# Kernel optimization log

Measured on AMD Instinct MI355X. Metric: run time of the kernel, lower is better.

## Reference

```python
import jax, jax.numpy as jnp
import numpy as np
from jax import lax

B, T, H, W = 4, 8, 14, 14
DIM, NH = 768, 8
HD = DIM // NH            # 96, head dim (= depthwise conv channels)
G = 1                     # global_embed_num
N = T * H * W + 1 + G     # 1570 tokens: [global, cls, spatial]
HID = 4 * DIM
BIG = 1.0e8


def ln(x, g, b, eps=1e-5):
    m = jnp.mean(x, axis=-1, keepdims=True)
    v = jnp.mean(jnp.square(x - m), axis=-1, keepdims=True)
    return (x - m) * jax.lax.rsqrt(v + eps) * g + b


def setup_inputs() -> dict:
    key = jax.random.key(0)
    ks = jax.random.split(key, 12)
    s = 0.02
    inp = {
        "x": jax.random.normal(ks[0], (B, N, DIM), jnp.float32),
        "t": T, "h": H, "w": W,
        "norm1_g": jnp.ones((DIM,), jnp.float32),
        "norm1_b": jnp.zeros((DIM,), jnp.float32),
        "qkv_w": jax.random.normal(ks[1], (3 * DIM, DIM), jnp.float32) * s,
        "qkv_b": jnp.zeros((3 * DIM,), jnp.float32),
        "conv_q": jax.random.normal(ks[2], (HD, 1, 3, 3, 3), jnp.float32) * 0.05,
        "nq_g": jnp.ones((HD,), jnp.float32), "nq_b": jnp.zeros((HD,), jnp.float32),
        "conv_k": jax.random.normal(ks[3], (HD, 1, 3, 3, 3), jnp.float32) * 0.05,
        "nk_g": jnp.ones((HD,), jnp.float32), "nk_b": jnp.zeros((HD,), jnp.float32),
        "conv_v": jax.random.normal(ks[4], (HD, 1, 3, 3, 3), jnp.float32) * 0.05,
        "nv_g": jnp.ones((HD,), jnp.float32), "nv_b": jnp.zeros((HD,), jnp.float32),
        "proj_w": jax.random.normal(ks[5], (DIM, DIM), jnp.float32) * s,
        "proj_b": jnp.zeros((DIM,), jnp.float32),
        "norm2_g": jnp.ones((DIM,), jnp.float32),
        "norm2_b": jnp.zeros((DIM,), jnp.float32),
        "fc1_w": jax.random.normal(ks[6], (HID, DIM), jnp.float32) * s,
        "fc1_b": jnp.zeros((HID,), jnp.float32),
        "fc2_w": jax.random.normal(ks[7], (DIM, HID), jnp.float32) * s,
        "fc2_b": jnp.zeros((DIM,), jnp.float32),
    }
    return inp


def _pool(tok, cw, g, b):
    # tok: [B, NH, N, HD] -> depthwise conv3d per head on spatial tokens, then LN
    glob, cls, body = tok[:, :, :G], tok[:, :, G:G + 1], tok[:, :, G + 1:]
    z = body.reshape(B * NH, T, H, W, HD).transpose(0, 4, 1, 2, 3)  # [BN, C, T, H, W]
    z = lax.conv_general_dilated(z, cw, window_strides=(1, 1, 1),
                                 padding=[(1, 1)] * 3, feature_group_count=HD,
                                 dimension_numbers=("NCDHW", "OIDHW", "NCDHW"))
    z = z.reshape(B, NH, HD, T * H * W).transpose(0, 1, 3, 2)       # [B, NH, L, HD]
    z = jnp.concatenate([glob, cls, z], axis=2)                     # splice cls then global
    return ln(z, g, b)


def reference(x, t, h, w, norm1_g, norm1_b, qkv_w, qkv_b,
              conv_q, nq_g, nq_b, conv_k, nk_g, nk_b, conv_v, nv_g, nv_b,
              proj_w, proj_b, norm2_g, norm2_b, fc1_w, fc1_b, fc2_w, fc2_b):
    scale = HD ** (-0.5)
    xn = ln(x, norm1_g, norm1_b)
    qkv = (xn @ qkv_w.T + qkv_b).reshape(B, N, 3, NH, HD)
    qkv = qkv.transpose(2, 0, 3, 1, 4)            # [3, B, NH, N, HD]
    q = _pool(qkv[0], conv_q, nq_g, nq_b)
    k = _pool(qkv[1], conv_k, nk_g, nk_b)
    v = _pool(qkv[2], conv_v, nv_g, nv_b)

    attn = jnp.einsum("bhnd,bhmd->bhnm", q, k) * scale
    # additive offset: BIG everywhere except diagonal and the global columns (rows >= G)
    eye = jnp.eye(N, dtype=attn.dtype)
    off2 = eye * BIG
    off2 = off2.at[G:, :G].set(BIG)
    offset = BIG - off2                            # [N, N]
    attn = jax.nn.softmax(attn - offset, axis=-1)

    o = jnp.einsum("bhnm,bhmd->bhnd", attn, v)     # [B, NH, N, HD]
    o = o.transpose(0, 2, 1, 3).reshape(B, N, DIM)
    o = o @ proj_w.T + proj_b

    x = x + o                                      # pool_skip is None -> identity skip
    x2 = ln(x, norm2_g, norm2_b)
    mlp = jax.nn.gelu(x2 @ fc1_w.T + fc1_b, approximate=False) @ fc2_w.T + fc2_b
    return x + mlp
```

## Files before the change

### kernel.cpp

```cpp
#include <hip/hip_runtime.h>
#include <hip/hip_bf16.h>
#include <cmath>

using bf16 = __hip_bfloat16;
using bf16x8_t = __attribute__((ext_vector_type(8))) short;
using f32x4_t  = __attribute__((ext_vector_type(4))) float;

constexpr int kT = 8;
constexpr int kDIM = 768, kNH = 8, kHD = 96;
constexpr int kN = 1570;
constexpr int kB = 4;
constexpr int kM = kB * kN;
constexpr int kBNH = kB * kNH;
constexpr long kPoolRows  = (long)kBNH * kN;
constexpr long kPoolElems = kPoolRows * kHD;

struct SegTab { const void* src[22]; long start[23]; };

__global__ void detect_kernel(const unsigned* __restrict__ probe,
                              unsigned* __restrict__ flag) {
  *flag = (probe[0] == 0x3F803F80u) ? 1u : 0u;
}

__global__ void convert_kernel(SegTab tab, bf16* __restrict__ cin,
                               const unsigned* __restrict__ flag, long chunks) {
  const bool isb = (*flag != 0u);
  const long stride = (long)gridDim.x * blockDim.x;
  for (long c = (long)blockIdx.x * blockDim.x + threadIdx.x; c < chunks; c += stride) {
    const long e8 = c * 8;
    int lo = 0, hi = 22;
    while (hi - lo > 1) { int mid = (lo + hi) >> 1; if (e8 >= tab.start[mid]) lo = mid; else hi = mid; }
    const long e = e8 - tab.start[lo];
    if (isb) {
      *(bf16x8_t*)(cin + e8) = *(const bf16x8_t*)((const unsigned short*)tab.src[lo] + e);
    } else {
      const float* s = (const float*)tab.src[lo] + e;
      float4 a = *(const float4*)s;
      float4 b = *(const float4*)(s + 4);
      bf16 r[8];
      r[0] = (bf16)a.x; r[1] = (bf16)a.y; r[2] = (bf16)a.z; r[3] = (bf16)a.w;
      r[4] = (bf16)b.x; r[5] = (bf16)b.y; r[6] = (bf16)b.z; r[7] = (bf16)b.w;
      *(bf16x8_t*)(cin + e8) = *(bf16x8_t*)r;
    }
  }
}

__device__ __forceinline__ void gload_lds16(const bf16* g, bf16* l) {
  __builtin_amdgcn_global_load_lds(
      (const __attribute__((address_space(1))) unsigned int*)g,
      (__attribute__((address_space(3))) unsigned int*)l, 16, 0, 0);
}

template<int EPI, int DUAL>
__launch_bounds__(256, 2)
__global__ void gemm_bt(const bf16* __restrict__ A, const bf16* __restrict__ Wt,
                        const bf16* __restrict__ bias, const bf16* __restrict__ res,
                        bf16* __restrict__ C, float* __restrict__ Cf,
                        const unsigned* __restrict__ flagp,
                        int M, int K, int Nout, int tiles_n)
{
  __shared__ bf16 shm[32768];
  const int tid  = threadIdx.x;
  const int lane = tid & 63;
  const int wv   = tid >> 6;
  const int wr   = wv >> 1, wc = wv & 1;

  const int nwg = gridDim.x;
  const int q8 = nwg >> 3, r8 = nwg & 7;
  const int xcd = blockIdx.x & 7, slot = blockIdx.x >> 3;
  const int base = (xcd < r8) ? xcd * (q8 + 1) : r8 * (q8 + 1) + (xcd - r8) * q8;
  const int lin = base + slot;
  const int grp = lin / (2 * tiles_n);
  const int rem = lin - grp * 2 * tiles_n;
  const long tile_m = (long)(grp * 2 + (rem & 1)) * 128;
  const long tile_n = (long)(rem >> 1) * 128;

  bool isb = true;
  if constexpr (DUAL) isb = (*flagp != 0u);

  f32x4_t zero = {0.f, 0.f, 0.f, 0.f};
  f32x4_t acc[4][4];
#pragma unroll
  for (int i = 0; i < 4; ++i)
#pragma unroll
    for (int j = 0; j < 4; ++j) acc[i][j] = zero;

  const int rbase = tid >> 3;
  const int g8 = (((tid & 7) ^ (rbase & 7))) * 8;
  const bf16* srcA[4];
  const bf16* srcB[4];
#pragma unroll
  for (int i = 0; i < 4; ++i) {
    long ar = tile_m + i * 32 + rbase; if (ar > M - 1) ar = M - 1;
    srcA[i] = A  + ar * K + g8;
    srcB[i] = Wt + (tile_n + i * 32 + rbase) * K + g8;
  }

  auto stage = [&](int kt, int buf) {
    const long koff = (long)kt << 6;
    bf16* ab = shm + buf * 8192;
    bf16* bp = shm + 16384 + buf * 8192;
#pragma unroll
    for (int i = 0; i < 4; ++i)
      gload_lds16(srcA[i] + koff, ab + i * 2048 + wv * 512);
#pragma unroll
    for (int i = 0; i < 4; ++i)
      gload_lds16(srcB[i] + koff, bp + i * 2048 + wv * 512);
  };

  const int qq = lane & 7;
  const int j0 = (((lane >> 4) ^ qq)) * 8;
  const int j1 = (((lane >> 4) ^ 4 ^ qq)) * 8;
  const int rA = wr * 64 + (lane & 15);
  const int rB = wc * 64 + (lane & 15);

  const int ksteps = K >> 6;
  stage(0, 0);
  stage(1, 1);
  asm volatile("s_waitcnt vmcnt(8)" ::: "memory");
  __builtin_amdgcn_s_barrier();

#define KSTEP(BUF, DOPF, PFKT)                                                 \
  {                                                                            \
    const bf16* ab = shm + (BUF) * 8192;                                       \
    const bf16* bp = shm + 16384 + (BUF) * 8192;                               \
    bf16x8_t a[4][2], bfr[4][2];                                               \
    _Pragma("unroll")                                                          \
    for (int m = 0; m < 4; ++m) {                                              \
      a[m][0]   = *(const bf16x8_t*)&ab[((rA + m * 16) << 6) + j0];            \
      a[m][1]   = *(const bf16x8_t*)&ab[((rA + m * 16) << 6) + j1];            \
      bfr[m][0] = *(const bf16x8_t*)&bp[((rB + m * 16) << 6) + j0];            \
      bfr[m][1] = *(const bf16x8_t*)&bp[((rB + m * 16) << 6) + j1];            \
    }                                                                          \
    asm volatile("s_waitcnt lgkmcnt(0)" ::: "memory");                         \
    __builtin_amdgcn_sched_barrier(0);                                         \
    __builtin_amdgcn_s_barrier();                                              \
    if (DOPF) stage((PFKT), (BUF));                                            \
    __builtin_amdgcn_s_setprio(1);                                             \
    _Pragma("unroll")                                                          \
    for (int m = 0; m < 4; ++m)                                                \
      _Pragma("unroll")                                                        \
      for (int n = 0; n < 4; ++n) {                                            \
        acc[m][n] = __builtin_amdgcn_mfma_f32_16x16x32_bf16(a[m][0], bfr[n][0], acc[m][n], 0, 0, 0); \
        acc[m][n] = __builtin_amdgcn_mfma_f32_16x16x32_bf16(a[m][1], bfr[n][1], acc[m][n], 0, 0, 0); \
      }                                                                        \
    __builtin_amdgcn_s_setprio(0);                                             \
    if (DOPF) { asm volatile("s_waitcnt vmcnt(8)" ::: "memory"); }             \
    else      { asm volatile("s_waitcnt vmcnt(0)" ::: "memory"); }             \
    __builtin_amdgcn_s_barrier();                                              \
  }

  for (int p = 0; p < ksteps; p += 2) {
    KSTEP(0, p + 2 < ksteps, p + 2)
    KSTEP(1, p + 3 < ksteps, p + 3)
  }
#undef KSTEP

  {
    const int colB = wc * 64 + (lane & 15);
    const int rowB = wr * 64 + ((lane >> 4) << 2);
#pragma unroll
    for (int n = 0; n < 4; ++n) {
      const int col = colB + n * 16;
      const float bv = (float)bias[tile_n + col];
#pragma unroll
      for (int m = 0; m < 4; ++m)
#pragma unroll
        for (int r = 0; r < 4; ++r)
          shm[(rowB + m * 16 + r) * 136 + col] = (bf16)(acc[m][n][r] + bv);
    }
  }
  __syncthreads();
#pragma unroll
  for (int c8 = 0; c8 < 8; ++c8) {
    const int chunk = tid + c8 * 256;
    const int row = chunk >> 4;
    const int colc = (chunk & 15) * 8;
    const long grow = tile_m + row;
    if (grow < M) {
      const bf16x8_t v8 = *(const bf16x8_t*)&shm[row * 136 + colc];
      const long gcol = tile_n + colc;
      float f[8];
#pragma unroll
      for (int j = 0; j < 8; ++j) {
        unsigned short u = (unsigned short)v8[j];
        f[j] = __uint_as_float((unsigned)u << 16);
      }
      if constexpr (EPI == 1) {
#pragma unroll
        for (int j = 0; j < 8; ++j) {
          const float v2 = f[j];
          const float zarg = 1.59576912160573f * v2 * (1.f + 0.044715f * v2 * v2);
          f[j] = v2 * __builtin_amdgcn_rcpf(1.f + __expf(-zarg));
        }
      } else if constexpr (EPI == 2) {
        const bf16x8_t rv = *(const bf16x8_t*)&res[grow * Nout + gcol];
#pragma unroll
        for (int j = 0; j < 8; ++j) {
          unsigned short u = (unsigned short)rv[j];
          f[j] += __uint_as_float((unsigned)u << 16);
        }
      }
      if (DUAL && !isb) {
        float4 s0 = {f[0], f[1], f[2], f[3]};
        float4 s1 = {f[4], f[5], f[6], f[7]};
        *(float4*)&Cf[grow * Nout + gcol] = s0;
        *(float4*)&Cf[grow * Nout + gcol + 4] = s1;
      } else {
        bf16 o8[8];
#pragma unroll
        for (int j = 0; j < 8; ++j) o8[j] = (bf16)f[j];
        *(bf16x8_t*)&C[grow * Nout + gcol] = *(bf16x8_t*)o8;
      }
    }
  }
}

__global__ void ln768_kernel(const bf16* __restrict__ x, const bf16* __restrict__ g,
                             const bf16* __restrict__ bta, bf16* __restrict__ y)
{
  const long row = blockIdx.x;
  const int tid = threadIdx.x;
  const bf16* xr = x + row * kDIM;
  float v[3];
  float s = 0.f, ss = 0.f;
#pragma unroll
  for (int i = 0; i < 3; ++i) {
    v[i] = (float)xr[tid + i * 256];
    s += v[i]; ss += v[i] * v[i];
  }
#pragma unroll
  for (int off = 32; off; off >>= 1) {
    s  += __shfl_xor(s, off);
    ss += __shfl_xor(ss, off);
  }
  __shared__ float red[8];
  const int wv = tid >> 6;
  if ((tid & 63) == 0) { red[wv] = s; red[4 + wv] = ss; }
  __syncthreads();
  s  = red[0] + red[1] + red[2] + red[3];
  ss = red[4] + red[5] + red[6] + red[7];
  const float mean = s * (1.f / kDIM);
  const float var  = ss * (1.f / kDIM) - mean * mean;
  const float rstd = rsqrtf(var + 1e-5f);
  bf16* yr = y + row * kDIM;
#pragma unroll
  for (int i = 0; i < 3; ++i) {
    const int c = tid + i * 256;
    yr[c] = (bf16)((v[i] - mean) * rstd * (float)g[c] + (float)bta[c]);
  }
}

__launch_bounds__(256, 2)
__global__ void convpool2_kernel(const bf16* __restrict__ qkv,
                                 const bf16* __restrict__ cwq,
                                 const bf16* __restrict__ cwk,
                                 const bf16* __restrict__ cwv,
                                 bf16* __restrict__ pool)
{
  __shared__ bf16 tile[3 * 256 * 40];
  const int t    = blockIdx.x;
  const int bh   = blockIdx.y;
  const int z    = blockIdx.z;
  const int s    = z / 3, cgrp = z - s * 3;
  const int tid  = threadIdx.x;
  const int b    = bh >> 3, h = bh & 7;

  const bf16* src0 = qkv + (long)(b * kN) * 2304 + s * kDIM + h * kHD + cgrp * 32;

  {
    f32x4_t z4 = {0.f, 0.f, 0.f, 0.f};
    for (int i = tid; i < 3840; i += 256)
      *(f32x4_t*)((char*)tile + (long)i * 16) = z4;
  }
  __syncthreads();

  for (int c = tid; c < 2352; c += 256) {
    const int slice = c / 784;
    const int rem   = c - slice * 784;
    const int p     = rem >> 2;
    const int seg   = rem & 3;
    const int tt    = t + slice - 1;
    if ((unsigned)tt < 8u) {
      const int y = p / 14, x = p - y * 14;
      const int n = 2 + tt * 196 + p;
      const bf16x8_t v = *(const bf16x8_t*)(src0 + (long)n * 2304 + seg * 8);
      *(bf16x8_t*)((char*)tile + ((long)(slice * 256 + (y + 1) * 16 + (x + 1)) * 40 + seg * 8) * 2) = v;
    }
  }

  const int dpair = tid & 15;
  const int pg    = tid >> 4;
  const int d0    = cgrp * 32 + dpair * 2;
  const bf16* cw  = (s == 0) ? cwq : (s == 1) ? cwk : cwv;
  float w0[27], w1[27];
#pragma unroll
  for (int i = 0; i < 27; ++i) {
    w0[i] = (float)cw[d0 * 27 + i];
    w1[i] = (float)cw[(d0 + 1) * 27 + i];
  }
  __syncthreads();

  bf16* out0 = pool + (long)s * kPoolElems + (long)bh * kN * kHD;
  for (int p = pg; p < 196; p += 16) {
    const int y = p / 14, x = p - y * 14;
    const char* bp = (const char*)tile + ((long)(y * 16 + x) * 40 + dpair * 2) * 2;
    float a0 = 0.f, a1 = 0.f;
#pragma unroll
    for (int dt = 0; dt < 3; ++dt)
#pragma unroll
      for (int dy = 0; dy < 3; ++dy)
#pragma unroll
        for (int dx = 0; dx < 3; ++dx) {
          const unsigned u = *(const unsigned*)(bp + dt * 20480 + dy * 1280 + dx * 80);
          const int i = (dt * 3 + dy) * 3 + dx;
          a0 = fmaf(__uint_as_float(u << 16), w0[i], a0);
          a1 = fmaf(__uint_as_float(u & 0xffff0000u), w1[i], a1);
        }
    const int n = 2 + t * 196 + p;
    bf16 r0 = (bf16)a0, r1 = (bf16)a1;
    unsigned pk = ((unsigned)*(unsigned short*)&r1 << 16) | *(unsigned short*)&r0;
    *(unsigned*)((char*)(out0 + (long)n * kHD + d0)) = pk;
  }
  if (t == 0 && tid < 64) {
    const int tok = tid >> 5, dd = tid & 31;
    out0[(long)tok * kHD + cgrp * 32 + dd] = src0[(long)tok * 2304 + dd];
  }
}

__global__ void ln96_kernel(bf16* __restrict__ pool,
                            const bf16* __restrict__ gq, const bf16* __restrict__ bq,
                            const bf16* __restrict__ gk, const bf16* __restrict__ bk,
                            const bf16* __restrict__ gv, const bf16* __restrict__ bv)
{
  const int z = blockIdx.y;
  bf16* buf = pool + (long)z * kPoolElems;
  const bf16* g  = (z == 0) ? gq : (z == 1) ? gk : gv;
  const bf16* be = (z == 0) ? bq : (z == 1) ? bk : bv;
  const long row = (long)blockIdx.x * 4 + (threadIdx.x >> 6);
  if (row >= kPoolRows) return;
  const int lane = threadIdx.x & 63;
  bf16* p = buf + row * kHD;
  float a0 = 0.f, a1 = 0.f;
  if (lane < 48) {
    a0 = (float)p[lane * 2];
    a1 = (float)p[lane * 2 + 1];
  }
  float sSum = a0 + a1, sSq = a0 * a0 + a1 * a1;
#pragma unroll
  for (int off = 32; off; off >>= 1) {
    sSum += __shfl_xor(sSum, off);
    sSq  += __shfl_xor(sSq, off);
  }
  const float mean = sSum * (1.f / 96);
  const float var  = sSq * (1.f / 96) - mean * mean;
  const float rstd = rsqrtf(var + 1e-5f);
  if (lane < 48) {
    p[lane * 2]     = (bf16)((a0 - mean) * rstd * (float)g[lane * 2]     + (float)be[lane * 2]);
    p[lane * 2 + 1] = (bf16)((a1 - mean) * rstd * (float)g[lane * 2 + 1] + (float)be[lane * 2 + 1]);
  }
}

__global__ void attn_kernel(const bf16* __restrict__ pool, bf16* __restrict__ o)
{
  const long idx = (long)blockIdx.x * 4 + (threadIdx.x >> 6);
  if (idx >= kPoolRows) return;
  const int bh = (int)(idx / kN);
  const int i  = (int)(idx - (long)bh * kN);
  const int lane = threadIdx.x & 63;
  const bf16* qrow  = pool + ((long)bh * kN + i) * kHD;
  const bf16* kbase = pool + kPoolElems + (long)bh * kN * kHD;
  const bf16* vbase = pool + 2 * kPoolElems + (long)bh * kN * kHD;
  float q0 = 0, q1 = 0, ki0 = 0, ki1 = 0, k00 = 0, k01 = 0;
  float vi0 = 0, vi1 = 0, v00 = 0, v01 = 0;
  if (lane < 48) {
    const int c = lane * 2;
    q0  = (float)qrow[c];                  q1  = (float)qrow[c + 1];
    ki0 = (float)kbase[(long)i * kHD + c]; ki1 = (float)kbase[(long)i * kHD + c + 1];
    k00 = (float)kbase[c];                 k01 = (float)kbase[c + 1];
    vi0 = (float)vbase[(long)i * kHD + c]; vi1 = (float)vbase[(long)i * kHD + c + 1];
    v00 = (float)vbase[c];                 v01 = (float)vbase[c + 1];
  }
  float ds = q0 * ki0 + q1 * ki1;
  float dg = q0 * k00 + q1 * k01;
#pragma unroll
  for (int off = 32; off; off >>= 1) {
    ds += __shfl_xor(ds, off);
    dg += __shfl_xor(dg, off);
  }
  float o0, o1;
  if (i == 0) { o0 = v00; o1 = v01; }
  else {
    const float scale = 0.10206207261596575f;
    const float l0 = dg * scale, li = ds * scale;
    const float mx = fmaxf(l0, li);
    const float e0 = __expf(l0 - mx), ei = __expf(li - mx);
    const float inv = 1.f / (e0 + ei);
    o0 = (e0 * v00 + ei * vi0) * inv;
    o1 = (e0 * v01 + ei * vi1) * inv;
  }
  if (lane < 48) {
    const int b = bh >> 3, h = bh & 7;
    bf16* orow = o + ((long)b * kN + i) * kDIM + h * kHD + lane * 2;
    orow[0] = (bf16)o0;
    orow[1] = (bf16)o1;
  }
}

extern "C" void kernel_launch(void* const* d_in, const int* in_sizes, int n_in,
                              void* d_out, int out_size, void* d_ws, size_t ws_size,
                              hipStream_t stream)
{
  const int map[22] = {0,4,5,6,7,8,9,10,11,12,13,14,15,16,17,18,19,20,21,22,23,24};

  char* ws = (char*)d_ws;
  unsigned* flag = (unsigned*)ws;

  size_t off = 256;
  auto take = [&](size_t bytes) {
    size_t r = off;
    off += (bytes + 255) & ~(size_t)255;
    return r;
  };

  SegTab tab;
  long total = 0;
  tab.start[0] = 0;
  for (int j = 0; j < 22; ++j) {
    tab.src[j] = d_in[map[j]];
    total += in_sizes[map[j]];
    tab.start[j + 1] = total;
  }

  bf16* cin = (bf16*)(ws + take((size_t)total * 2));

  bf16* cp[22];
  { long acc = 0;
    for (int j = 0; j < 22; ++j) { cp[j] = cin + acc; acc += in_sizes[map[j]]; } }
  bf16* x_c    = cp[0];
  bf16* n1g_c  = cp[1],  *n1b_c = cp[2];
  bf16* qkvw_c = cp[3],  *qkvb_c = cp[4];
  bf16* cwq_c  = cp[5],  *nqg_c = cp[6],  *nqb_c = cp[7];
  bf16* cwk_c  = cp[8],  *nkg_c = cp[9],  *nkb_c = cp[10];
  bf16* cwv_c  = cp[11], *nvg_c = cp[12], *nvb_c = cp[13];
  bf16* projw_c = cp[14], *projb_c = cp[15];
  bf16* n2g_c  = cp[16], *n2b_c = cp[17];
  bf16* fc1w_c = cp[18], *fc1b_c = cp[19];
  bf16* fc2w_c = cp[20], *fc2b_c = cp[21];

  bf16* qkv  = (bf16*)(ws + take(38584320));
  bf16* xn   = (bf16*)(ws + take(9646080));
  bf16* pool = (bf16*)(ws + take(28938240));
  bf16* x1   = (bf16*)(ws + take(9646080));
  bf16* o   = xn;
  bf16* h1  = qkv;
  bf16* x2n = pool;

  bf16*  out_b = (bf16*)d_out;
  float* out_f = (float*)d_out;

  detect_kernel<<<1, 1, 0, stream>>>((const unsigned*)d_in[4], flag);
  convert_kernel<<<2048, 256, 0, stream>>>(tab, cin, flag, total / 8);

  ln768_kernel<<<kM, 256, 0, stream>>>(x_c, n1g_c, n1b_c, xn);
  gemm_bt<0,0><<<50 * 18, 256, 0, stream>>>(xn, qkvw_c, qkvb_c, nullptr, qkv, nullptr, nullptr, kM, 768, 2304, 18);
  convpool2_kernel<<<dim3(kT, kBNH, 9), 256, 0, stream>>>(qkv, cwq_c, cwk_c, cwv_c, pool);
  ln96_kernel<<<dim3((int)((kPoolRows + 3) / 4), 3), 256, 0, stream>>>(pool, nqg_c, nqb_c, nkg_c, nkb_c, nvg_c, nvb_c);
  attn_kernel<<<(int)((kPoolRows + 3) / 4), 256, 0, stream>>>(pool, o);
  gemm_bt<2,0><<<50 * 6, 256, 0, stream>>>(o, projw_c, projb_c, x_c, x1, nullptr, nullptr, kM, 768, 768, 6);
  ln768_kernel<<<kM, 256, 0, stream>>>(x1, n2g_c, n2b_c, x2n);
  gemm_bt<1,0><<<50 * 24, 256, 0, stream>>>(x2n, fc1w_c, fc1b_c, nullptr, h1, nullptr, nullptr, kM, 768, 3072, 24);
  gemm_bt<2,1><<<50 * 6, 256, 0, stream>>>(h1, fc2w_c, fc2b_c, x1, out_b, out_f, flag, kM, 3072, 768, 6);
}
```

Before: 281.1 us.

## Use 256x128 GEMM tiles with 8 waves and split conv-pool into 16-channel groups

The bf16 GEMM moves from a 128x128 tile with 4 waves to a 256x128 tile with 512 threads. This is meant to halve how often the weight tiles are reloaded and to raise the MFMA work done per LDS byte. An odd-tile fallback mapping handles the 25 row tiles. The depthwise conv-pool kernel now processes 16 channels per block instead of 32, with a smaller LDS tile and higher occupancy bounds, to spread work over more blocks. The trade-off is that the proj and fc2 GEMMs now launch only 150 blocks, which may leave compute units idle.

```diff
diff --git a/kernel.cpp b/kernel.cpp
--- a/kernel.cpp
+++ b/kernel.cpp
@@ -52,28 +52,38 @@
 }
 
 template<int EPI, int DUAL>
-__launch_bounds__(256, 2)
+__launch_bounds__(512, 2)
 __global__ void gemm_bt(const bf16* __restrict__ A, const bf16* __restrict__ Wt,
                         const bf16* __restrict__ bias, const bf16* __restrict__ res,
                         bf16* __restrict__ C, float* __restrict__ Cf,
                         const unsigned* __restrict__ flagp,
                         int M, int K, int Nout, int tiles_n)
 {
-  __shared__ bf16 shm[32768];
+  __shared__ bf16 shm[49152];
   const int tid  = threadIdx.x;
   const int lane = tid & 63;
   const int wv   = tid >> 6;
-  const int wr   = wv >> 1, wc = wv & 1;
+  const int wr   = wv & 3, wc = wv >> 2;
 
   const int nwg = gridDim.x;
+  const int tiles_m = nwg / tiles_n;
   const int q8 = nwg >> 3, r8 = nwg & 7;
   const int xcd = blockIdx.x & 7, slot = blockIdx.x >> 3;
   const int base = (xcd < r8) ? xcd * (q8 + 1) : r8 * (q8 + 1) + (xcd - r8) * q8;
   const int lin = base + slot;
-  const int grp = lin / (2 * tiles_n);
-  const int rem = lin - grp * 2 * tiles_n;
-  const long tile_m = (long)(grp * 2 + (rem & 1)) * 128;
-  const long tile_n = (long)(rem >> 1) * 128;
+  const int paired = (tiles_m & ~1) * tiles_n;
+  int tmi, tni;
+  if (lin < paired) {
+    const int grp = lin / (2 * tiles_n);
+    const int rem = lin - grp * 2 * tiles_n;
+    tmi = grp * 2 + (rem & 1);
+    tni = rem >> 1;
+  } else {
+    tmi = tiles_m - 1;
+    tni = lin - paired;
+  }
+  const long tile_m = (long)tmi * 256;
+  const long tile_n = (long)tni * 128;
 
   bool isb = true;
   if constexpr (DUAL) isb = (*flagp != 0u);
@@ -85,52 +95,51 @@
 #pragma unroll
     for (int j = 0; j < 4; ++j) acc[i][j] = zero;
 
-  const int rbase = tid >> 3;
-  const int g8 = (((tid & 7) ^ (rbase & 7))) * 8;
-  const bf16* srcA[4];
-  const bf16* srcB[4];
+  const int rb = tid >> 3;
+  const int g8 = (((tid & 7) ^ (rb & 7))) * 8;
+  const bf16* sA[4];
+  const bf16* sB[2];
 #pragma unroll
   for (int i = 0; i < 4; ++i) {
-    long ar = tile_m + i * 32 + rbase; if (ar > M - 1) ar = M - 1;
-    srcA[i] = A  + ar * K + g8;
-    srcB[i] = Wt + (tile_n + i * 32 + rbase) * K + g8;
-  }
+    long ar = tile_m + rb + i * 64; if (ar > M - 1) ar = M - 1;
+    sA[i] = A + ar * K + g8;
+  }
+#pragma unroll
+  for (int i = 0; i < 2; ++i)
+    sB[i] = Wt + (tile_n + rb + i * 64) * K + g8;
 
   auto stage = [&](int kt, int buf) {
     const long koff = (long)kt << 6;
-    bf16* ab = shm + buf * 8192;
-    bf16* bp = shm + 16384 + buf * 8192;
 #pragma unroll
     for (int i = 0; i < 4; ++i)
-      gload_lds16(srcA[i] + koff, ab + i * 2048 + wv * 512);
-#pragma unroll
-    for (int i = 0; i < 4; ++i)
-      gload_lds16(srcB[i] + koff, bp + i * 2048 + wv * 512);
+      gload_lds16(sA[i] + koff, shm + buf * 16384 + i * 4096 + tid * 8);
+#pragma unroll
+    for (int i = 0; i < 2; ++i)
+      gload_lds16(sB[i] + koff, shm + 32768 + buf * 8192 + i * 4096 + tid * 8);
   };
 
-  const int qq = lane & 7;
-  const int j0 = (((lane >> 4) ^ qq)) * 8;
-  const int j1 = (((lane >> 4) ^ 4 ^ qq)) * 8;
-  const int rA = wr * 64 + (lane & 15);
-  const int rB = wc * 64 + (lane & 15);
+  const int j0 = (((lane >> 4) ^ (lane & 7))) * 8;
+  const int j1 = ((((lane >> 4) ^ 4)) ^ (lane & 7)) * 8;
+  const int rA0 = wr * 64 + (lane & 15);
+  const int rB0 = wc * 64 + (lane & 15);
 
   const int ksteps = K >> 6;
   stage(0, 0);
   stage(1, 1);
-  asm volatile("s_waitcnt vmcnt(8)" ::: "memory");
+  asm volatile("s_waitcnt vmcnt(6)" ::: "memory");
   __builtin_amdgcn_s_barrier();
 
 #define KSTEP(BUF, DOPF, PFKT)                                                 \
   {                                                                            \
-    const bf16* ab = shm + (BUF) * 8192;                                       \
-    const bf16* bp = shm + 16384 + (BUF) * 8192;                               \
+    const bf16* ab = shm + (BUF) * 16384;                                      \
+    const bf16* bp = shm + 32768 + (BUF) * 8192;                               \
     bf16x8_t a[4][2], bfr[4][2];                                               \
     _Pragma("unroll")                                                          \
     for (int m = 0; m < 4; ++m) {                                              \
-      a[m][0]   = *(const bf16x8_t*)&ab[((rA + m * 16) << 6) + j0];            \
-      a[m][1]   = *(const bf16x8_t*)&ab[((rA + m * 16) << 6) + j1];            \
-      bfr[m][0] = *(const bf16x8_t*)&bp[((rB + m * 16) << 6) + j0];            \
-      bfr[m][1] = *(const bf16x8_t*)&bp[((rB + m * 16) << 6) + j1];            \
+      a[m][0]   = *(const bf16x8_t*)&ab[((rA0 + m * 16) << 6) + j0];           \
+      a[m][1]   = *(const bf16x8_t*)&ab[((rA0 + m * 16) << 6) + j1];           \
+      bfr[m][0] = *(const bf16x8_t*)&bp[((rB0 + m * 16) << 6) + j0];           \
+      bfr[m][1] = *(const bf16x8_t*)&bp[((rB0 + m * 16) << 6) + j1];           \
     }                                                                          \
     asm volatile("s_waitcnt lgkmcnt(0)" ::: "memory");                         \
     __builtin_amdgcn_sched_barrier(0);                                         \
@@ -145,7 +154,7 @@
         acc[m][n] = __builtin_amdgcn_mfma_f32_16x16x32_bf16(a[m][1], bfr[n][1], acc[m][n], 0, 0, 0); \
       }                                                                        \
     __builtin_amdgcn_s_setprio(0);                                             \
-    if (DOPF) { asm volatile("s_waitcnt vmcnt(8)" ::: "memory"); }             \
+    if (DOPF) { asm volatile("s_waitcnt vmcnt(6)" ::: "memory"); }             \
     else      { asm volatile("s_waitcnt vmcnt(0)" ::: "memory"); }             \
     __builtin_amdgcn_s_barrier();                                              \
   }
@@ -157,23 +166,23 @@
 #undef KSTEP
 
   {
-    const int colB = wc * 64 + (lane & 15);
-    const int rowB = wr * 64 + ((lane >> 4) << 2);
+    const int cB = wc * 64 + (lane & 15);
+    const int rB = wr * 64 + ((lane >> 4) << 2);
 #pragma unroll
     for (int n = 0; n < 4; ++n) {
-      const int col = colB + n * 16;
+      const int col = cB + n * 16;
       const float bv = (float)bias[tile_n + col];
 #pragma unroll
       for (int m = 0; m < 4; ++m)
 #pragma unroll
         for (int r = 0; r < 4; ++r)
-          shm[(rowB + m * 16 + r) * 136 + col] = (bf16)(acc[m][n][r] + bv);
+          shm[(rB + m * 16 + r) * 136 + col] = (bf16)(acc[m][n][r] + bv);
     }
   }
   __syncthreads();
 #pragma unroll
-  for (int c8 = 0; c8 < 8; ++c8) {
-    const int chunk = tid + c8 * 256;
+  for (int it = 0; it < 8; ++it) {
+    const int chunk = tid + it * 512;
     const int row = chunk >> 4;
     const int colc = (chunk & 15) * 8;
     const long grow = tile_m + row;
@@ -251,47 +260,47 @@
   }
 }
 
-__launch_bounds__(256, 2)
-__global__ void convpool2_kernel(const bf16* __restrict__ qkv,
+__launch_bounds__(256, 4)
+__global__ void convpool3_kernel(const bf16* __restrict__ qkv,
                                  const bf16* __restrict__ cwq,
                                  const bf16* __restrict__ cwk,
                                  const bf16* __restrict__ cwv,
                                  bf16* __restrict__ pool)
 {
-  __shared__ bf16 tile[3 * 256 * 40];
+  __shared__ bf16 tile[3 * 256 * 16];
   const int t    = blockIdx.x;
   const int bh   = blockIdx.y;
   const int z    = blockIdx.z;
-  const int s    = z / 3, cgrp = z - s * 3;
+  const int s    = z / 6, cgrp = z - s * 6;
   const int tid  = threadIdx.x;
   const int b    = bh >> 3, h = bh & 7;
 
-  const bf16* src0 = qkv + (long)(b * kN) * 2304 + s * kDIM + h * kHD + cgrp * 32;
+  const bf16* src0 = qkv + (long)(b * kN) * 2304 + s * kDIM + h * kHD + cgrp * 16;
 
   {
     f32x4_t z4 = {0.f, 0.f, 0.f, 0.f};
-    for (int i = tid; i < 3840; i += 256)
+    for (int i = tid; i < 3072; i += 256)
       *(f32x4_t*)((char*)tile + (long)i * 16) = z4;
   }
   __syncthreads();
 
-  for (int c = tid; c < 2352; c += 256) {
-    const int slice = c / 784;
-    const int rem   = c - slice * 784;
-    const int p     = rem >> 2;
-    const int seg   = rem & 3;
+  for (int c = tid; c < 1176; c += 256) {
+    const int slice = c / 392;
+    const int rem   = c - slice * 392;
+    const int p     = rem >> 1;
+    const int seg   = rem & 1;
     const int tt    = t + slice - 1;
     if ((unsigned)tt < 8u) {
       const int y = p / 14, x = p - y * 14;
       const int n = 2 + tt * 196 + p;
       const bf16x8_t v = *(const bf16x8_t*)(src0 + (long)n * 2304 + seg * 8);
-      *(bf16x8_t*)((char*)tile + ((long)(slice * 256 + (y + 1) * 16 + (x + 1)) * 40 + seg * 8) * 2) = v;
+      *(bf16x8_t*)&tile[slice * 4096 + ((y + 1) * 16 + (x + 1)) * 16 + seg * 8] = v;
     }
   }
 
-  const int dpair = tid & 15;
-  const int pg    = tid >> 4;
-  const int d0    = cgrp * 32 + dpair * 2;
+  const int dpair = tid & 7;
+  const int pg    = tid >> 3;
+  const int d0    = cgrp * 16 + dpair * 2;
   const bf16* cw  = (s == 0) ? cwq : (s == 1) ? cwk : cwv;
   float w0[27], w1[27];
 #pragma unroll
@@ -302,9 +311,9 @@
   __syncthreads();
 
   bf16* out0 = pool + (long)s * kPoolElems + (long)bh * kN * kHD;
-  for (int p = pg; p < 196; p += 16) {
+  for (int p = pg; p < 196; p += 32) {
     const int y = p / 14, x = p - y * 14;
-    const char* bp = (const char*)tile + ((long)(y * 16 + x) * 40 + dpair * 2) * 2;
+    const char* bp = (const char*)tile + ((y * 16 + x) * 16 + dpair * 2) * 2;
     float a0 = 0.f, a1 = 0.f;
 #pragma unroll
     for (int dt = 0; dt < 3; ++dt)
@@ -312,7 +321,7 @@
       for (int dy = 0; dy < 3; ++dy)
 #pragma unroll
         for (int dx = 0; dx < 3; ++dx) {
-          const unsigned u = *(const unsigned*)(bp + dt * 20480 + dy * 1280 + dx * 80);
+          const unsigned u = *(const unsigned*)(bp + dt * 8192 + dy * 512 + dx * 32);
           const int i = (dt * 3 + dy) * 3 + dx;
           a0 = fmaf(__uint_as_float(u << 16), w0[i], a0);
           a1 = fmaf(__uint_as_float(u & 0xffff0000u), w1[i], a1);
@@ -322,9 +331,9 @@
     unsigned pk = ((unsigned)*(unsigned short*)&r1 << 16) | *(unsigned short*)&r0;
     *(unsigned*)((char*)(out0 + (long)n * kHD + d0)) = pk;
   }
-  if (t == 0 && tid < 64) {
-    const int tok = tid >> 5, dd = tid & 31;
-    out0[(long)tok * kHD + cgrp * 32 + dd] = src0[(long)tok * 2304 + dd];
+  if (t == 0 && tid < 32) {
+    const int tok = tid >> 4, dd = tid & 15;
+    out0[(long)tok * kHD + cgrp * 16 + dd] = src0[(long)tok * 2304 + dd];
   }
 }
 
@@ -463,12 +472,12 @@
   convert_kernel<<<2048, 256, 0, stream>>>(tab, cin, flag, total / 8);
 
   ln768_kernel<<<kM, 256, 0, stream>>>(x_c, n1g_c, n1b_c, xn);
-  gemm_bt<0,0><<<50 * 18, 256, 0, stream>>>(xn, qkvw_c, qkvb_c, nullptr, qkv, nullptr, nullptr, kM, 768, 2304, 18);
-  convpool2_kernel<<<dim3(kT, kBNH, 9), 256, 0, stream>>>(qkv, cwq_c, cwk_c, cwv_c, pool);
+  gemm_bt<0,0><<<25 * 18, 512, 0, stream>>>(xn, qkvw_c, qkvb_c, nullptr, qkv, nullptr, nullptr, kM, 768, 2304, 18);
+  convpool3_kernel<<<dim3(kT, kBNH, 18), 256, 0, stream>>>(qkv, cwq_c, cwk_c, cwv_c, pool);
   ln96_kernel<<<dim3((int)((kPoolRows + 3) / 4), 3), 256, 0, stream>>>(pool, nqg_c, nqb_c, nkg_c, nkb_c, nvg_c, nvb_c);
   attn_kernel<<<(int)((kPoolRows + 3) / 4), 256, 0, stream>>>(pool, o);
-  gemm_bt<2,0><<<50 * 6, 256, 0, stream>>>(o, projw_c, projb_c, x_c, x1, nullptr, nullptr, kM, 768, 768, 6);
+  gemm_bt<2,0><<<25 * 6, 512, 0, stream>>>(o, projw_c, projb_c, x_c, x1, nullptr, nullptr, kM, 768, 768, 6);
   ln768_kernel<<<kM, 256, 0, stream>>>(x1, n2g_c, n2b_c, x2n);
-  gemm_bt<1,0><<<50 * 24, 256, 0, stream>>>(x2n, fc1w_c, fc1b_c, nullptr, h1, nullptr, nullptr, kM, 768, 3072, 24);
-  gemm_bt<2,1><<<50 * 6, 256, 0, stream>>>(h1, fc2w_c, fc2b_c, x1, out_b, out_f, flag, kM, 3072, 768, 6);
-}
+  gemm_bt<1,0><<<25 * 24, 512, 0, stream>>>(x2n, fc1w_c, fc1b_c, nullptr, h1, nullptr, nullptr, kM, 768, 3072, 24);
+  gemm_bt<2,1><<<25 * 6, 512, 0, stream>>>(h1, fc2w_c, fc2b_c, x1, out_b, out_f, flag, kM, 3072, 768, 6);
+}
```

Result: no change. 275.7 us (-1.9%).
